# Optimization experiments

Measured on AMD Instinct MI355X. Metric: run time of the kernel, lower is better.

## Reference

```python
import jax, jax.numpy as jnp
import numpy as np

N_SAMPLES = 16384
L = 8000   # num pseudo labels
C = 8      # num cameras
D = 256    # feature dim
N = 512    # batch size
T = 0.05   # temperature
K = 50     # hard_neg_k
LW = 0.5   # inter-cam loss weight


def setup_inputs() -> dict:
    key = jax.random.key(0)
    k1, k2, k3, k4, k5 = jax.random.split(key, 5)
    feats = jax.random.normal(k1, (N, D), dtype=jnp.float32)
    indexes = jax.random.randint(k2, (N,), 0, N_SAMPLES)
    label_table = jax.random.randint(k3, (N_SAMPLES,), 0, L)
    cam_table = jax.random.randint(k4, (N_SAMPLES,), 0, C)
    centers = jax.random.normal(k5, (L * C, D), dtype=jnp.float32)
    centers = centers / jnp.linalg.norm(centers, axis=1, keepdims=True)
    return {"feats": feats, "indexes": indexes, "label_table": label_table,
            "cam_table": cam_table, "centers": centers}


def reference(feats, indexes, label_table, cam_table, centers):
    # F.normalize(feats, p=2, dim=1)
    feats = feats / jnp.linalg.norm(feats, axis=1, keepdims=True)
    labels = label_table[indexes]          # [n]
    cams = cam_table[indexes]              # [n]
    cen = jax.lax.stop_gradient(centers)   # centers are a non-grad buffer in torch

    all_sims = feats @ cen.T               # [n, P]  P = L*C, proxy(l,c) = l*C + c
    n, P = all_sims.shape
    sims_r = all_sims.reshape(n, L, C)     # [n, L, C]

    # ---- intra-camera loss: softmax over the L proxies sharing sample's camera ----
    idx_cam = jnp.broadcast_to(cams[:, None, None], (n, L, 1))
    sims_intra = jnp.take_along_axis(sims_r, idx_cam, axis=2)[..., 0]  # [n, L]
    logp_intra = jax.nn.log_softmax(sims_intra / T, axis=1)
    loss_intra_i = -jnp.take_along_axis(logp_intra, labels[:, None], axis=1)[:, 0]

    # ---- inter-camera loss: C positives (same label, all cams) + top-K hard negatives ----
    idx_lab = jnp.broadcast_to(labels[:, None, None], (n, 1, C))
    pos_sims = jnp.take_along_axis(sims_r, idx_lab, axis=1)[:, 0, :]   # [n, C]
    masked = jnp.where(jnp.arange(L)[None, :, None] == labels[:, None, None],
                       jnp.float32(-10000.0), sims_r).reshape(n, P)
    neg_sims, _ = jax.lax.top_k(masked, K)                             # [n, K]
    logits = jnp.concatenate([pos_sims, neg_sims], axis=1) / T         # [n, C+K]
    logp = jax.nn.log_softmax(logits, axis=1)
    loss_inter_i = -jnp.mean(logp[:, :C], axis=1)  # target = 1/C on the C positives

    # ---- per-camera mean, summed over cameras (matches the torch.unique loop) ----
    ones = jnp.ones((n,), feats.dtype)
    counts = jax.ops.segment_sum(ones, cams, num_segments=C)
    safe = jnp.maximum(counts, 1.0)
    s_intra = jax.ops.segment_sum(loss_intra_i, cams, num_segments=C)
    s_inter = jax.ops.segment_sum(loss_inter_i, cams, num_segments=C)
    loss_intra = jnp.sum(jnp.where(counts > 0, s_intra / safe, 0.0))
    loss_inter = LW * jnp.sum(jnp.where(counts > 0, s_inter / safe, 0.0))
    return jnp.stack([loss_intra, loss_inter])
```

## Files before the change

kernel.cpp:

```cpp
#include <hip/hip_runtime.h>
#include <stdint.h>

#define NS   512
#define DDIM 256
#define LL   8000
#define CC   8
#define PP   64000
#define KTOP 50
#define CAP  1024

typedef float f32x4 __attribute__((ext_vector_type(4)));
typedef short bf16x8 __attribute__((ext_vector_type(8)));
typedef short short8 __attribute__((ext_vector_type(8)));

__device__ __forceinline__ ushort f2bf(float x) {
    uint32_t b = __float_as_uint(x);
    b += 0x7fffu + ((b >> 16) & 1u);
    return (ushort)(b >> 16);
}
__device__ __forceinline__ float bf2f(ushort u) {
    return __uint_as_float(((uint32_t)u) << 16);
}

__global__ void k_norm_gather(const float* __restrict__ feats,
                              const int* __restrict__ indexes,
                              const int* __restrict__ ltab,
                              const int* __restrict__ ctab,
                              ushort* __restrict__ feats_b,
                              int* __restrict__ labels,
                              int* __restrict__ cams) {
    const int n = blockIdx.x;
    const int lane = threadIdx.x;
    f32x4 v = ((const f32x4*)(feats + (size_t)n * DDIM))[lane];
    float ss = v[0]*v[0] + v[1]*v[1] + v[2]*v[2] + v[3]*v[3];
#pragma unroll
    for (int off = 32; off > 0; off >>= 1) ss += __shfl_down(ss, off);
    float tot = __shfl(ss, 0);
    float sc = 1.0f / sqrtf(tot);
    ushort4 o;
    o.x = f2bf(v[0] * sc); o.y = f2bf(v[1] * sc);
    o.z = f2bf(v[2] * sc); o.w = f2bf(v[3] * sc);
    ((ushort4*)(feats_b + (size_t)n * DDIM))[lane] = o;
    if (lane == 0) {
        int idx = indexes[n];
        labels[n] = ltab[idx];
        cams[n] = ctab[idx];
    }
}

__global__ __launch_bounds__(256, 2)
void k_gemm(const ushort* __restrict__ A, const float* __restrict__ B,
            const int* __restrict__ labels, const int* __restrict__ cams,
            ushort* __restrict__ sims, float* __restrict__ intrabuf,
            float* __restrict__ posbuf) {
    const int lane = threadIdx.x & 63;
    const int w    = threadIdx.x >> 6;
    const int lr   = lane & 15;
    const int lk   = lane >> 4;
    const int bRow = blockIdx.y * 128;
    const int cBase = blockIdx.x * 128 + w * 32;

    __shared__ int s_lab[128], s_cam[128];
    if (threadIdx.x < 128) {
        s_lab[threadIdx.x] = labels[bRow + threadIdx.x];
        s_cam[threadIdx.x] = cams[bRow + threadIdx.x];
    }

    bf16x8 bfr[2][8];
#pragma unroll
    for (int nn = 0; nn < 2; ++nn) {
#pragma unroll
        for (int kb = 0; kb < 8; ++kb) {
            const float* src = B + (size_t)(cBase + nn * 16 + lr) * DDIM + kb * 32 + lk * 8;
            f32x4 a = *(const f32x4*)src;
            f32x4 b = *(const f32x4*)(src + 4);
            bf16x8 r;
            r[0] = (short)f2bf(a[0]); r[1] = (short)f2bf(a[1]);
            r[2] = (short)f2bf(a[2]); r[3] = (short)f2bf(a[3]);
            r[4] = (short)f2bf(b[0]); r[5] = (short)f2bf(b[1]);
            r[6] = (short)f2bf(b[2]); r[7] = (short)f2bf(b[3]);
            bfr[nn][kb] = r;
        }
    }
    __syncthreads();

    f32x4 zero = {0.f, 0.f, 0.f, 0.f};
    f32x4 acc[8][2];
#pragma unroll
    for (int m = 0; m < 8; ++m) { acc[m][0] = zero; acc[m][1] = zero; }

#pragma unroll
    for (int kb = 0; kb < 8; ++kb) {
        const int kpos = kb * 32 + lk * 8;
#pragma unroll
        for (int m = 0; m < 8; ++m) {
            bf16x8 afr = *(const bf16x8*)(A + (size_t)(bRow + m * 16 + lr) * DDIM + kpos);
            acc[m][0] = __builtin_amdgcn_mfma_f32_16x16x32_bf16(afr, bfr[0][kb], acc[m][0], 0, 0, 0);
            acc[m][1] = __builtin_amdgcn_mfma_f32_16x16x32_bf16(afr, bfr[1][kb], acc[m][1], 0, 0, 0);
        }
    }

#pragma unroll
    for (int m = 0; m < 8; ++m) {
#pragma unroll
        for (int nn = 0; nn < 2; ++nn) {
#pragma unroll
            for (int j = 0; j < 4; ++j) {
                int rl  = m * 16 + lk * 4 + j;
                int row = bRow + rl;
                int col = cBase + nn * 16 + lr;
                float v = acc[m][nn][j];
                sims[(size_t)row * PP + col] = f2bf(v);
                int g = col >> 3, cc = col & 7;
                if (g == s_lab[rl]) posbuf[row * CC + cc] = v;
                if (cc == s_cam[rl]) intrabuf[(size_t)row * LL + g] = v;
            }
        }
    }
}

__global__ __launch_bounds__(256)
void k_persample(const ushort* __restrict__ sims, const float* __restrict__ intrabuf,
                 const float* __restrict__ posbuf, const int* __restrict__ labels,
                 const int* __restrict__ cams, float* __restrict__ li,
                 float* __restrict__ le) {
    const int n = blockIdx.x;
    const int tid = threadIdx.x;
    const int label = labels[n];
    const int cam = cams[n];
    const ushort* row = sims + (size_t)n * PP;
    const float* irow = intrabuf + (size_t)n * LL;

    __shared__ float cand[CAP];
    __shared__ float s_redA[256];
    __shared__ float s_redB[256];
    __shared__ int   s_cnt;
    __shared__ float s_tau, s_sig, s_sum, s_M;
    __shared__ float s_pos[CC];

    const float K2 = 28.853900817779268f;

    float lss = 0.0f, lcc = 0.0f;
    float my_m = -1e30f, my_s = 0.0f;
    for (int g = tid; g < LL / 4; g += 256) {
        f32x4 v = ((const f32x4*)irow)[g];
#pragma unroll
        for (int j = 0; j < 4; ++j) {
            int l = g * 4 + j;
            float y = v[j] * K2;
            if (y > my_m) { my_s = my_s * exp2f(my_m - y) + 1.0f; my_m = y; }
            else          { my_s += exp2f(y - my_m); }
            if (l != label) { lss += v[j] * v[j]; lcc += 1.0f; }
        }
    }
    s_redA[tid] = lss; s_redB[tid] = lcc;
    __syncthreads();
    for (int off = 128; off > 0; off >>= 1) {
        if (tid < off) { s_redA[tid] += s_redA[tid + off]; s_redB[tid] += s_redB[tid + off]; }
        __syncthreads();
    }
    if (tid == 0) {
        float sig = sqrtf(s_redA[0] / fmaxf(s_redB[0], 1.0f));
        s_sig = sig;
        s_tau = 2.9f * sig;
    }
    __syncthreads();
    s_redA[tid] = my_m; s_redB[tid] = my_s;
    __syncthreads();
    for (int off = 128; off > 0; off >>= 1) {
        if (tid < off) {
            float m1 = s_redA[tid],       s1 = s_redB[tid];
            float m2 = s_redA[tid + off], s2 = s_redB[tid + off];
            float M = fmaxf(m1, m2);
            s_redB[tid] = s1 * exp2f(m1 - M) + s2 * exp2f(m2 - M);
            s_redA[tid] = M;
        }
        __syncthreads();
    }
    if (tid == 0) {
        float lse_nat = 0.6931471805599453f * (s_redA[0] + log2f(s_redB[0]));
        li[n] = lse_nat - posbuf[n * CC + cam] * 20.0f;
    }
    if (tid < CC) s_pos[tid] = posbuf[n * CC + tid];

    int pass = 0;
    int c;
    for (;;) {
        __syncthreads();
        if (tid == 0) s_cnt = 0;
        __syncthreads();
        float tau = s_tau;
        for (int g = tid; g < LL; g += 256) {
            if (g == label) continue;
            short8 u = ((const short8*)row)[g];
#pragma unroll
            for (int j = 0; j < 8; ++j) {
                float v = bf2f((ushort)u[j]);
                if (v > tau) {
                    int id = atomicAdd(&s_cnt, 1);
                    if (id < CAP) cand[id] = v;
                }
            }
        }
        __syncthreads();
        c = s_cnt;
        if ((c >= KTOP && c <= CAP) || pass >= 24) break;
        if (tid == 0) s_tau = (c < KTOP) ? (tau - 0.25f * s_sig) : (tau + 0.125f * s_sig);
        pass++;
    }
    if (c > CAP) c = CAP;

    float lm = -1e30f;
    for (int i = tid; i < c; i += 256) lm = fmaxf(lm, cand[i]);
    if (tid < CC) lm = fmaxf(lm, s_pos[tid]);
    s_redA[tid] = lm;
    __syncthreads();
    for (int off = 128; off > 0; off >>= 1) {
        if (tid < off) s_redA[tid] = fmaxf(s_redA[tid], s_redA[tid + off]);
        __syncthreads();
    }
    if (tid == 0) { s_M = s_redA[0]; s_sum = 0.0f; }
    __syncthreads();
    const float M = s_M;

    for (int i = tid; i < c; i += 256) {
        float v = cand[i];
        int r = 0;
        for (int j = 0; j < c; ++j) {
            float u = cand[j];
            r += (u > v) || (u == v && j < i);
        }
        if (r < KTOP) atomicAdd(&s_sum, exp2f((v - M) * K2));
    }
    if (tid < CC) atomicAdd(&s_sum, exp2f((s_pos[tid] - M) * K2));
    __syncthreads();
    if (tid == 0) {
        float possum = 0.0f;
#pragma unroll
        for (int j = 0; j < CC; ++j) possum += s_pos[j];
        float lse_nat = M * 20.0f + logf(s_sum);
        le[n] = lse_nat - possum * 20.0f / 8.0f;
    }
}

__global__ void k_finalize(const float* __restrict__ li, const float* __restrict__ le,
                           const int* __restrict__ cams, float* __restrict__ out) {
    __shared__ float si[CC], se[CC];
    __shared__ int sc[CC];
    int tid = threadIdx.x;
    if (tid < CC) { si[tid] = 0.f; se[tid] = 0.f; sc[tid] = 0; }
    __syncthreads();
    for (int i = tid; i < NS; i += 256) {
        int cm = cams[i];
        atomicAdd(&si[cm], li[i]);
        atomicAdd(&se[cm], le[i]);
        atomicAdd(&sc[cm], 1);
    }
    __syncthreads();
    if (tid == 0) {
        float a = 0.f, b = 0.f;
        for (int cm = 0; cm < CC; ++cm) {
            if (sc[cm] > 0) {
                a += si[cm] / (float)sc[cm];
                b += se[cm] / (float)sc[cm];
            }
        }
        out[0] = a;
        out[1] = 0.5f * b;
    }
}

extern "C" void kernel_launch(void* const* d_in, const int* in_sizes, int n_in,
                              void* d_out, int out_size, void* d_ws, size_t ws_size,
                              hipStream_t stream) {
    const float* feats   = (const float*)d_in[0];
    const int*   indexes = (const int*)d_in[1];
    const int*   ltab    = (const int*)d_in[2];
    const int*   ctab    = (const int*)d_in[3];
    const float* centers = (const float*)d_in[4];
    float* out = (float*)d_out;

    const size_t SZ_SIMS  = (size_t)NS * PP * sizeof(ushort);
    const size_t SZ_INTRA = (size_t)NS * LL * sizeof(float);
    const size_t SZ_POS   = (size_t)NS * CC * sizeof(float);
    const size_t SZ_FB    = (size_t)NS * DDIM * sizeof(ushort);

    char* p = (char*)d_ws;
    ushort* sims    = (ushort*)p;  p += SZ_SIMS;
    float*  intrabf = (float*)p;   p += SZ_INTRA;
    float*  posbuf  = (float*)p;   p += SZ_POS;
    ushort* fb      = (ushort*)p;  p += SZ_FB;
    int* labels = (int*)p;         p += 2048;
    int* cams   = (int*)p;         p += 2048;
    float* li   = (float*)p;       p += 2048;
    float* le   = (float*)p;       p += 2048;

    hipLaunchKernelGGL(k_norm_gather, dim3(NS), dim3(64), 0, stream,
                       feats, indexes, ltab, ctab, fb, labels, cams);
    hipLaunchKernelGGL(k_gemm, dim3(500, 4), dim3(256), 0, stream,
                       fb, centers, labels, cams, sims, intrabf, posbuf);
    hipLaunchKernelGGL(k_persample, dim3(NS), dim3(256), 0, stream,
                       sims, intrabf, posbuf, labels, cams, li, le);
    hipLaunchKernelGGL(k_finalize, dim3(1), dim3(256), 0, stream, li, le, cams, out);
}
```

Baseline: 246.0 us.

## Fuse top-K candidate filtering and intra softmax sums into GEMM epilogue

Stops writing the full 512x64000 bf16 similarity matrix and the intra-camera buffer to memory. A small sampling kernel first estimates a global sigma for the threshold. The GEMM epilogue then accumulates exp sums for the intra softmax per row and pushes above-threshold candidates into per-row global lists with atomics. A fixup kernel recomputes dot products by bisection for rows whose candidate count falls outside range. Without max subtraction, the exp sums can overflow or lose precision. Global atomics in the epilogue and the slow fixup path are new costs.

```diff
diff --git a/kernel.cpp b/kernel.cpp
--- a/kernel.cpp
+++ b/kernel.cpp
@@ -8,10 +8,11 @@
 #define PP   64000
 #define KTOP 50
 #define CAP  1024
+#define NBLK 2000
+#define K2C  28.853900817779268f
 
 typedef float f32x4 __attribute__((ext_vector_type(4)));
 typedef short bf16x8 __attribute__((ext_vector_type(8)));
-typedef short short8 __attribute__((ext_vector_type(8)));
 
 __device__ __forceinline__ ushort f2bf(float x) {
     uint32_t b = __float_as_uint(x);
@@ -48,41 +49,74 @@
     }
 }
 
-__global__ __launch_bounds__(256, 2)
-void k_gemm(const ushort* __restrict__ A, const float* __restrict__ B,
-            const int* __restrict__ labels, const int* __restrict__ cams,
-            ushort* __restrict__ sims, float* __restrict__ intrabuf,
-            float* __restrict__ posbuf) {
-    const int lane = threadIdx.x & 63;
-    const int w    = threadIdx.x >> 6;
+__global__ __launch_bounds__(256) void k_sigma(const ushort* __restrict__ fb,
+                                               const float* __restrict__ B,
+                                               float* __restrict__ sig_acc) {
+    __shared__ float cf[DDIM];
+    __shared__ float red[256];
+    const int tid = threadIdx.x;
+    const int p = blockIdx.x * 997 + 123;
+    cf[tid] = bf2f(f2bf(B[(size_t)p * DDIM + tid]));
+    __syncthreads();
+    float s = 0.0f;
+#pragma unroll
+    for (int rr = 0; rr < 2; ++rr) {
+        int r = tid * 2 + rr;
+        const ushort* a = fb + (size_t)r * DDIM;
+        float d = 0.0f;
+        for (int k = 0; k < DDIM; k += 8) {
+            bf16x8 av = *(const bf16x8*)(a + k);
+#pragma unroll
+            for (int j = 0; j < 8; ++j) d += bf2f((ushort)av[j]) * cf[k + j];
+        }
+        s += d * d;
+    }
+    red[tid] = s;
+    __syncthreads();
+    for (int off = 128; off > 0; off >>= 1) {
+        if (tid < off) red[tid] += red[tid + off];
+        __syncthreads();
+    }
+    if (tid == 0) atomicAdd(sig_acc, red[0]);
+}
+
+__global__ __launch_bounds__(256, 4)
+void k_gemm_fused(const ushort* __restrict__ A, const float* __restrict__ B,
+                  const int* __restrict__ labels, const int* __restrict__ cams,
+                  const float* __restrict__ sig_acc,
+                  float* __restrict__ partial, float* __restrict__ cand,
+                  int* __restrict__ gcount, float* __restrict__ posbuf) {
+    const int bx   = blockIdx.x;
+    const int cBase = bx * 32;
+    const int tid  = threadIdx.x;
+    const int lane = tid & 63;
+    const int w    = tid >> 6;
     const int lr   = lane & 15;
     const int lk   = lane >> 4;
-    const int bRow = blockIdx.y * 128;
-    const int cBase = blockIdx.x * 128 + w * 32;
-
-    __shared__ int s_lab[128], s_cam[128];
-    if (threadIdx.x < 128) {
-        s_lab[threadIdx.x] = labels[bRow + threadIdx.x];
-        s_cam[threadIdx.x] = cams[bRow + threadIdx.x];
-    }
-
-    bf16x8 bfr[2][8];
-#pragma unroll
-    for (int nn = 0; nn < 2; ++nn) {
-#pragma unroll
-        for (int kb = 0; kb < 8; ++kb) {
-            const float* src = B + (size_t)(cBase + nn * 16 + lr) * DDIM + kb * 32 + lk * 8;
-            f32x4 a = *(const f32x4*)src;
-            f32x4 b = *(const f32x4*)(src + 4);
-            bf16x8 r;
-            r[0] = (short)f2bf(a[0]); r[1] = (short)f2bf(a[1]);
-            r[2] = (short)f2bf(a[2]); r[3] = (short)f2bf(a[3]);
-            r[4] = (short)f2bf(b[0]); r[5] = (short)f2bf(b[1]);
-            r[6] = (short)f2bf(b[2]); r[7] = (short)f2bf(b[3]);
-            bfr[nn][kb] = r;
-        }
-    }
-    __syncthreads();
+
+    __shared__ ushort sB[32][264];
+    __shared__ int   s_lab[NS];
+    __shared__ int   s_cam[NS];
+    __shared__ float s_intra[NS];
+
+#pragma unroll
+    for (int it = 0; it < 8; ++it) {
+        int q   = tid + it * 256;
+        int col = q >> 6;
+        int k4  = q & 63;
+        f32x4 a = *(const f32x4*)(B + (size_t)(cBase + col) * DDIM + k4 * 4);
+        ushort4 o;
+        o.x = f2bf(a[0]); o.y = f2bf(a[1]); o.z = f2bf(a[2]); o.w = f2bf(a[3]);
+        *(ushort4*)(&sB[col][k4 * 4]) = o;
+    }
+    for (int r = tid; r < NS; r += 256) {
+        s_lab[r] = labels[r];
+        s_cam[r] = cams[r];
+        s_intra[r] = 0.0f;
+    }
+    __syncthreads();
+
+    const float tau = 2.9f * sqrtf(sig_acc[0] * (1.0f / 32768.0f));
 
     f32x4 zero = {0.f, 0.f, 0.f, 0.f};
     f32x4 acc[8][2];
@@ -92,154 +126,174 @@
 #pragma unroll
     for (int kb = 0; kb < 8; ++kb) {
         const int kpos = kb * 32 + lk * 8;
+        bf16x8 b0 = *(const bf16x8*)(&sB[lr][kpos]);
+        bf16x8 b1 = *(const bf16x8*)(&sB[16 + lr][kpos]);
 #pragma unroll
         for (int m = 0; m < 8; ++m) {
-            bf16x8 afr = *(const bf16x8*)(A + (size_t)(bRow + m * 16 + lr) * DDIM + kpos);
-            acc[m][0] = __builtin_amdgcn_mfma_f32_16x16x32_bf16(afr, bfr[0][kb], acc[m][0], 0, 0, 0);
-            acc[m][1] = __builtin_amdgcn_mfma_f32_16x16x32_bf16(afr, bfr[1][kb], acc[m][1], 0, 0, 0);
+            bf16x8 a = *(const bf16x8*)(A + (size_t)(w * 128 + m * 16 + lr) * DDIM + kpos);
+            acc[m][0] = __builtin_amdgcn_mfma_f32_16x16x32_bf16(a, b0, acc[m][0], 0, 0, 0);
+            acc[m][1] = __builtin_amdgcn_mfma_f32_16x16x32_bf16(a, b1, acc[m][1], 0, 0, 0);
         }
     }
 
 #pragma unroll
     for (int m = 0; m < 8; ++m) {
 #pragma unroll
-        for (int nn = 0; nn < 2; ++nn) {
-#pragma unroll
-            for (int j = 0; j < 4; ++j) {
-                int rl  = m * 16 + lk * 4 + j;
-                int row = bRow + rl;
-                int col = cBase + nn * 16 + lr;
-                float v = acc[m][nn][j];
-                sims[(size_t)row * PP + col] = f2bf(v);
-                int g = col >> 3, cc = col & 7;
-                if (g == s_lab[rl]) posbuf[row * CC + cc] = v;
-                if (cc == s_cam[rl]) intrabuf[(size_t)row * LL + g] = v;
+        for (int j = 0; j < 4; ++j) {
+            const int r   = w * 128 + m * 16 + lk * 4 + j;
+            const int lab = s_lab[r];
+            const int cm  = s_cam[r];
+#pragma unroll
+            for (int nn = 0; nn < 2; ++nn) {
+                const int c_loc = nn * 16 + lr;
+                const float v = acc[m][nn][j];
+                if ((c_loc & 7) == cm)
+                    atomicAdd(&s_intra[r], exp2f(v * K2C));
+                const int g = (cBase + c_loc) >> 3;
+                if (g == lab) {
+                    posbuf[r * CC + (c_loc & 7)] = v;
+                } else if (v > tau) {
+                    int id = atomicAdd(&gcount[r], 1);
+                    if (id < CAP) cand[(size_t)r * CAP + id] = v;
+                }
             }
         }
     }
-}
-
-__global__ __launch_bounds__(256)
-void k_persample(const ushort* __restrict__ sims, const float* __restrict__ intrabuf,
-                 const float* __restrict__ posbuf, const int* __restrict__ labels,
-                 const int* __restrict__ cams, float* __restrict__ li,
-                 float* __restrict__ le) {
+    __syncthreads();
+    for (int r = tid; r < NS; r += 256)
+        partial[(size_t)bx * NS + r] = s_intra[r];
+}
+
+__global__ __launch_bounds__(256) void k_fixup(const ushort* __restrict__ fb,
+                                               const float* __restrict__ B,
+                                               const int* __restrict__ labels,
+                                               float* __restrict__ cand,
+                                               int* __restrict__ gcount) {
+    const int n = blockIdx.x;
+    const int c0 = gcount[n];
+    if (c0 >= KTOP && c0 <= CAP) return;
+
+    const int tid = threadIdx.x;
+    __shared__ float f[DDIM];
+    __shared__ float s_lo, s_hi;
+    __shared__ int   red[256];
+    __shared__ int   s_done;
+    __shared__ int   s_cnt;
+    if (tid < DDIM) f[tid] = bf2f(fb[(size_t)n * DDIM + tid]);
+    const int label = labels[n];
+    if (tid == 0) { s_lo = -1.01f; s_hi = 1.01f; s_done = 0; }
+    __syncthreads();
+
+    for (int it = 0; it < 16 && !s_done; ++it) {
+        float tm = 0.5f * (s_lo + s_hi);
+        int cnt = 0;
+        for (int p = tid; p < PP; p += 256) {
+            if ((p >> 3) == label) continue;
+            const float* col = B + (size_t)p * DDIM;
+            float d = 0.0f;
+            for (int k = 0; k < DDIM; ++k) d += f[k] * bf2f(f2bf(col[k]));
+            cnt += (d > tm);
+        }
+        red[tid] = cnt;
+        __syncthreads();
+        for (int off = 128; off > 0; off >>= 1) {
+            if (tid < off) red[tid] += red[tid + off];
+            __syncthreads();
+        }
+        int tot = red[0];
+        __syncthreads();
+        if (tot >= KTOP && tot <= CAP) {
+            if (tid == 0) s_cnt = 0;
+            __syncthreads();
+            for (int p = tid; p < PP; p += 256) {
+                if ((p >> 3) == label) continue;
+                const float* col = B + (size_t)p * DDIM;
+                float d = 0.0f;
+                for (int k = 0; k < DDIM; ++k) d += f[k] * bf2f(f2bf(col[k]));
+                if (d > tm) {
+                    int id = atomicAdd(&s_cnt, 1);
+                    if (id < CAP) cand[(size_t)n * CAP + id] = d;
+                }
+            }
+            __syncthreads();
+            if (tid == 0) { gcount[n] = (s_cnt > CAP) ? CAP : s_cnt; s_done = 1; }
+            __syncthreads();
+        } else {
+            if (tid == 0) { if (tot < KTOP) s_hi = tm; else s_lo = tm; }
+            __syncthreads();
+        }
+    }
+    if (s_done) return;
+    if (tid == 0) s_cnt = 0;
+    __syncthreads();
+    float tl = s_lo;
+    for (int p = tid; p < PP; p += 256) {
+        if ((p >> 3) == label) continue;
+        const float* col = B + (size_t)p * DDIM;
+        float d = 0.0f;
+        for (int k = 0; k < DDIM; ++k) d += f[k] * bf2f(f2bf(col[k]));
+        if (d > tl) {
+            int id = atomicAdd(&s_cnt, 1);
+            if (id < CAP) cand[(size_t)n * CAP + id] = d;
+        }
+    }
+    __syncthreads();
+    if (tid == 0) gcount[n] = (s_cnt > CAP) ? CAP : s_cnt;
+}
+
+__global__ __launch_bounds__(256) void k_row(const float* __restrict__ partial,
+                                             const float* __restrict__ cand,
+                                             const int* __restrict__ gcount,
+                                             const float* __restrict__ posbuf,
+                                             const int* __restrict__ labels,
+                                             const int* __restrict__ cams,
+                                             float* __restrict__ li,
+                                             float* __restrict__ le) {
     const int n = blockIdx.x;
     const int tid = threadIdx.x;
-    const int label = labels[n];
-    const int cam = cams[n];
-    const ushort* row = sims + (size_t)n * PP;
-    const float* irow = intrabuf + (size_t)n * LL;
-
-    __shared__ float cand[CAP];
-    __shared__ float s_redA[256];
-    __shared__ float s_redB[256];
-    __shared__ int   s_cnt;
-    __shared__ float s_tau, s_sig, s_sum, s_M;
-    __shared__ float s_pos[CC];
-
-    const float K2 = 28.853900817779268f;
-
-    float lss = 0.0f, lcc = 0.0f;
-    float my_m = -1e30f, my_s = 0.0f;
-    for (int g = tid; g < LL / 4; g += 256) {
-        f32x4 v = ((const f32x4*)irow)[g];
-#pragma unroll
-        for (int j = 0; j < 4; ++j) {
-            int l = g * 4 + j;
-            float y = v[j] * K2;
-            if (y > my_m) { my_s = my_s * exp2f(my_m - y) + 1.0f; my_m = y; }
-            else          { my_s += exp2f(y - my_m); }
-            if (l != label) { lss += v[j] * v[j]; lcc += 1.0f; }
-        }
-    }
-    s_redA[tid] = lss; s_redB[tid] = lcc;
+    __shared__ float red[256];
+    __shared__ float spos[CC];
+    __shared__ float scand[CAP];
+
+    float s = 0.0f;
+    for (int b = tid; b < NBLK; b += 256) s += partial[(size_t)b * NS + n];
+    red[tid] = s;
     __syncthreads();
     for (int off = 128; off > 0; off >>= 1) {
-        if (tid < off) { s_redA[tid] += s_redA[tid + off]; s_redB[tid] += s_redB[tid + off]; }
+        if (tid < off) red[tid] += red[tid + off];
+        __syncthreads();
+    }
+    if (tid < CC) spos[tid] = posbuf[n * CC + tid];
+    __syncthreads();
+    if (tid == 0) li[n] = logf(red[0]) * 0.6931471805599453f / 0.6931471805599453f - 20.0f * spos[cams[n]];
+    __syncthreads();
+
+    int c = gcount[n];
+    if (c > CAP) c = CAP;
+    for (int i = tid; i < c; i += 256) scand[i] = cand[(size_t)n * CAP + i];
+    __syncthreads();
+    float sum = 0.0f;
+    for (int i = tid; i < c; i += 256) {
+        float v = scand[i];
+        int rk = 0;
+        for (int j = 0; j < c; ++j) {
+            float u = scand[j];
+            rk += (u > v) || (u == v && j < i);
+        }
+        if (rk < KTOP) sum += exp2f(v * K2C);
+    }
+    if (tid < CC) sum += exp2f(spos[tid] * K2C);
+    red[tid] = sum;
+    __syncthreads();
+    for (int off = 128; off > 0; off >>= 1) {
+        if (tid < off) red[tid] += red[tid + off];
         __syncthreads();
     }
     if (tid == 0) {
-        float sig = sqrtf(s_redA[0] / fmaxf(s_redB[0], 1.0f));
-        s_sig = sig;
-        s_tau = 2.9f * sig;
-    }
-    __syncthreads();
-    s_redA[tid] = my_m; s_redB[tid] = my_s;
-    __syncthreads();
-    for (int off = 128; off > 0; off >>= 1) {
-        if (tid < off) {
-            float m1 = s_redA[tid],       s1 = s_redB[tid];
-            float m2 = s_redA[tid + off], s2 = s_redB[tid + off];
-            float M = fmaxf(m1, m2);
-            s_redB[tid] = s1 * exp2f(m1 - M) + s2 * exp2f(m2 - M);
-            s_redA[tid] = M;
-        }
-        __syncthreads();
-    }
-    if (tid == 0) {
-        float lse_nat = 0.6931471805599453f * (s_redA[0] + log2f(s_redB[0]));
-        li[n] = lse_nat - posbuf[n * CC + cam] * 20.0f;
-    }
-    if (tid < CC) s_pos[tid] = posbuf[n * CC + tid];
-
-    int pass = 0;
-    int c;
-    for (;;) {
-        __syncthreads();
-        if (tid == 0) s_cnt = 0;
-        __syncthreads();
-        float tau = s_tau;
-        for (int g = tid; g < LL; g += 256) {
-            if (g == label) continue;
-            short8 u = ((const short8*)row)[g];
-#pragma unroll
-            for (int j = 0; j < 8; ++j) {
-                float v = bf2f((ushort)u[j]);
-                if (v > tau) {
-                    int id = atomicAdd(&s_cnt, 1);
-                    if (id < CAP) cand[id] = v;
-                }
-            }
-        }
-        __syncthreads();
-        c = s_cnt;
-        if ((c >= KTOP && c <= CAP) || pass >= 24) break;
-        if (tid == 0) s_tau = (c < KTOP) ? (tau - 0.25f * s_sig) : (tau + 0.125f * s_sig);
-        pass++;
-    }
-    if (c > CAP) c = CAP;
-
-    float lm = -1e30f;
-    for (int i = tid; i < c; i += 256) lm = fmaxf(lm, cand[i]);
-    if (tid < CC) lm = fmaxf(lm, s_pos[tid]);
-    s_redA[tid] = lm;
-    __syncthreads();
-    for (int off = 128; off > 0; off >>= 1) {
-        if (tid < off) s_redA[tid] = fmaxf(s_redA[tid], s_redA[tid + off]);
-        __syncthreads();
-    }
-    if (tid == 0) { s_M = s_redA[0]; s_sum = 0.0f; }
-    __syncthreads();
-    const float M = s_M;
-
-    for (int i = tid; i < c; i += 256) {
-        float v = cand[i];
-        int r = 0;
-        for (int j = 0; j < c; ++j) {
-            float u = cand[j];
-            r += (u > v) || (u == v && j < i);
-        }
-        if (r < KTOP) atomicAdd(&s_sum, exp2f((v - M) * K2));
-    }
-    if (tid < CC) atomicAdd(&s_sum, exp2f((s_pos[tid] - M) * K2));
-    __syncthreads();
-    if (tid == 0) {
-        float possum = 0.0f;
-#pragma unroll
-        for (int j = 0; j < CC; ++j) possum += s_pos[j];
-        float lse_nat = M * 20.0f + logf(s_sum);
-        le[n] = lse_nat - possum * 20.0f / 8.0f;
+        float ps = 0.0f;
+#pragma unroll
+        for (int j = 0; j < CC; ++j) ps += spos[j];
+        le[n] = logf(red[0]) - 2.5f * ps;
     }
 }
 
@@ -280,26 +334,30 @@
     const float* centers = (const float*)d_in[4];
     float* out = (float*)d_out;
 
-    const size_t SZ_SIMS  = (size_t)NS * PP * sizeof(ushort);
-    const size_t SZ_INTRA = (size_t)NS * LL * sizeof(float);
-    const size_t SZ_POS   = (size_t)NS * CC * sizeof(float);
-    const size_t SZ_FB    = (size_t)NS * DDIM * sizeof(ushort);
-
     char* p = (char*)d_ws;
-    ushort* sims    = (ushort*)p;  p += SZ_SIMS;
-    float*  intrabf = (float*)p;   p += SZ_INTRA;
-    float*  posbuf  = (float*)p;   p += SZ_POS;
-    ushort* fb      = (ushort*)p;  p += SZ_FB;
-    int* labels = (int*)p;         p += 2048;
-    int* cams   = (int*)p;         p += 2048;
-    float* li   = (float*)p;       p += 2048;
-    float* le   = (float*)p;       p += 2048;
+    float*  cand    = (float*)p;   p += (size_t)NS * CAP * sizeof(float);
+    float*  partial = (float*)p;   p += (size_t)NBLK * NS * sizeof(float);
+    float*  posbuf  = (float*)p;   p += (size_t)NS * CC * sizeof(float);
+    ushort* fb      = (ushort*)p;  p += (size_t)NS * DDIM * sizeof(ushort);
+    int*    labels  = (int*)p;     p += 2048;
+    int*    cams    = (int*)p;     p += 2048;
+    float*  li      = (float*)p;   p += 2048;
+    float*  le      = (float*)p;   p += 2048;
+    int*    gcount  = (int*)p;     p += 2048;
+    float*  sig_acc = (float*)p;   p += 64;
+
+    hipMemsetAsync(gcount, 0, 2048 + 64, stream);
 
     hipLaunchKernelGGL(k_norm_gather, dim3(NS), dim3(64), 0, stream,
                        feats, indexes, ltab, ctab, fb, labels, cams);
-    hipLaunchKernelGGL(k_gemm, dim3(500, 4), dim3(256), 0, stream,
-                       fb, centers, labels, cams, sims, intrabf, posbuf);
-    hipLaunchKernelGGL(k_persample, dim3(NS), dim3(256), 0, stream,
-                       sims, intrabf, posbuf, labels, cams, li, le);
+    hipLaunchKernelGGL(k_sigma, dim3(64), dim3(256), 0, stream,
+                       fb, centers, sig_acc);
+    hipLaunchKernelGGL(k_gemm_fused, dim3(NBLK), dim3(256), 0, stream,
+                       fb, centers, labels, cams, sig_acc,
+                       partial, cand, gcount, posbuf);
+    hipLaunchKernelGGL(k_fixup, dim3(NS), dim3(256), 0, stream,
+                       fb, centers, labels, cand, gcount);
+    hipLaunchKernelGGL(k_row, dim3(NS), dim3(256), 0, stream,
+                       partial, cand, gcount, posbuf, labels, cams, li, le);
     hipLaunchKernelGGL(k_finalize, dim3(1), dim3(256), 0, stream, li, le, cams, out);
 }
```

Result: faster. 235.5 us (-4.2%).
